# Performance work log

Hardware: AMD Instinct MI355X
Metric: run time of the kernel (lower is better)

Reference implementation:

```python
import jax, jax.numpy as jnp
import numpy as np

B, C, D, H, W = 4, 64, 32, 64, 64
S, NH = 8, 4
HD = C // NH


def setup_inputs() -> dict:
    key = jax.random.key(0)
    ks = jax.random.split(key, 8)
    sc = 0.05
    return {
        "x": jax.random.normal(ks[0], (B, C, D, H, W), jnp.float32),
        "slot_init": jax.random.normal(ks[1], (1, C, S), jnp.float32),
        "slot_proj_w": jax.random.normal(ks[2], (C, C), jnp.float32) * sc,
        "slot_proj_b": jnp.zeros((C,), jnp.float32),
        "ln_g": jnp.ones((C,), jnp.float32),
        "ln_b": jnp.zeros((C,), jnp.float32),
        "in_proj_w": jax.random.normal(ks[3], (3 * C, C), jnp.float32) * sc,
        "in_proj_b": jnp.zeros((3 * C,), jnp.float32),
        "out_proj_w": jax.random.normal(ks[4], (C, C), jnp.float32) * sc,
        "out_proj_b": jnp.zeros((C,), jnp.float32),
        "feat_w": jax.random.normal(ks[5], (C, C), jnp.float32) * sc,
        "feat_b": jnp.zeros((C,), jnp.float32),
        "s2f_w": jax.random.normal(ks[6], (C, C), jnp.float32) * sc,
        "s2f_b": jnp.zeros((C,), jnp.float32),
    }


def _l2norm(v, axis):
    # F.normalize: v / max(||v||, eps)
    n = jnp.sqrt(jnp.sum(v * v, axis=axis, keepdims=True))
    return v / jnp.maximum(n, 1e-12)


def reference(x, slot_init, slot_proj_w, slot_proj_b, ln_g, ln_b,
              in_proj_w, in_proj_b, out_proj_w, out_proj_b,
              feat_w, feat_b, s2f_w, s2f_b):
    b, c, d, h, w = x.shape
    n = d * h * w
    x_flat = x.reshape(b, c, n)                                  # (b,c,N)
    slots = jnp.broadcast_to(slot_init, (b, c, S))               # (b,c,S)

    # ---- slot update: cosine-sim cross attention over N ----
    x_norm = _l2norm(x_flat, 1)
    slots_norm = _l2norm(slots, 1)
    sim = jnp.einsum('bcs,bcn->bsn', slots_norm, x_norm)         # (b,S,N)
    attn = jax.nn.softmax(sim, axis=2)
    updates = jnp.einsum('bcn,bsn->bsc', x_flat, attn)           # (b,S,c)
    slots_t = updates @ slot_proj_w.T + slot_proj_b              # (b,S,c)

    # ---- LayerNorm(channels) then tiny MHSA over S=8 slots ----
    mu = jnp.mean(slots_t, axis=-1, keepdims=True)
    var = jnp.mean((slots_t - mu) ** 2, axis=-1, keepdims=True)
    sn = (slots_t - mu) / jnp.sqrt(var + 1e-5) * ln_g + ln_b     # (b,S,c)

    qkv = sn @ in_proj_w.T + in_proj_b                           # (b,S,3c)
    q, k, v = jnp.split(qkv, 3, axis=-1)
    def heads(t):
        return t.reshape(b, S, NH, HD).transpose(0, 2, 1, 3)     # (b,H,S,hd)
    q, k, v = heads(q), heads(k), heads(v)
    scores = jnp.einsum('bhqd,bhkd->bhqk', q, k) / jnp.sqrt(jnp.float32(HD))
    a = jax.nn.softmax(scores, axis=-1)
    o = jnp.einsum('bhqk,bhkd->bhqd', a, v).transpose(0, 2, 1, 3).reshape(b, S, c)
    o = o @ out_proj_w.T + out_proj_b
    slots_t = slots_t + o                                        # (b,S,c)

    # ---- feature broadcast: 1x1x1 conv + slot->feature attention ----
    feat_flat = jnp.einsum('oc,bcn->bon', feat_w, x_flat) + feat_b[None, :, None]
    slots_feat = slots_t @ s2f_w.T + s2f_b                       # (b,S,c)
    sim2 = jnp.einsum('bsc,bcn->bsn', slots_feat, feat_flat)
    attn2 = jax.nn.softmax(sim2, axis=1)                         # softmax over slots
    out = jnp.einsum('bsc,bsn->bcn', slots_t, attn2)             # (b,c,N)
    return out.reshape(b, c, d, h, w) + x
```

## Files before the change

### kernel.cpp

```cpp
#include <hip/hip_runtime.h>
#include <hip/hip_bf16.h>

#define BB   4
#define CC   64
#define SS   8
#define NN   (32*64*64)
#define NH_  4
#define HD_  16
#define TA   128
#define BPA  128
#define NTB  8

typedef __attribute__((ext_vector_type(8))) short bf16x8;
typedef __attribute__((ext_vector_type(4))) float f32x4;

__device__ __forceinline__ unsigned short f2b(float f) {
    union { float f; unsigned u; } v; v.f = f;
    unsigned r = v.u + 0x7FFFu + ((v.u >> 16) & 1u);
    return (unsigned short)(r >> 16);
}
__device__ __forceinline__ unsigned bfpack(float a, float b) {
    union { float f; unsigned u; } x, y; x.f = a; y.f = b;
    unsigned ra = (x.u + 0x7FFFu + ((x.u >> 16) & 1u)) >> 16;
    unsigned rb = (y.u + 0x7FFFu + ((y.u >> 16) & 1u)) & 0xFFFF0000u;
    return ra | rb;
}

__global__ __launch_bounds__(256) void k_precomp(
    const float* __restrict__ slot_init,
    const float* __restrict__ s2fw, const float* __restrict__ s2fb,
    const float* __restrict__ fw, const float* __restrict__ fb,
    float* __restrict__ M, float* __restrict__ g0v,
    float* __restrict__ hv, float* __restrict__ h0,
    float* __restrict__ snT_ws)
{
    const int tid = threadIdx.x;
    if (blockIdx.x < 16) {
        const int cp = blockIdx.x*4 + (tid >> 6);
        const int c  = tid & 63;
        float acc = 0.f;
        #pragma unroll 8
        for (int o = 0; o < CC; ++o)
            acc += s2fw[o*CC + cp] * fw[o*CC + c];
        M[cp*CC + c] = acc;
    } else if (blockIdx.x == 16) {
        if (tid < 64) {
            float acc = 0.f;
            #pragma unroll 8
            for (int o = 0; o < CC; ++o) acc += s2fb[o] * fw[o*CC + tid];
            g0v[tid] = acc;
        } else if (tid < 128) {
            const int cp = tid - 64;
            float acc = 0.f;
            #pragma unroll 8
            for (int o = 0; o < CC; ++o) acc += s2fw[o*CC + cp] * fb[o];
            hv[cp] = acc;
        } else if (tid == 128) {
            float acc = 0.f;
            for (int o = 0; o < CC; ++o) acc += s2fb[o] * fb[o];
            *h0 = acc;
        }
    } else {
        __shared__ float nrm[SS];
        if (tid < 64) {
            const int s = tid & 7, ch = tid >> 3;
            float p = 0.f;
            #pragma unroll
            for (int j = 0; j < 8; ++j) {
                float v = slot_init[(ch*8 + j)*SS + s];
                p += v*v;
            }
            p += __shfl_xor(p, 8); p += __shfl_xor(p, 16); p += __shfl_xor(p, 32);
            if (tid < 8) nrm[s] = fmaxf(sqrtf(p), 1e-12f);
        }
        __syncthreads();
        for (int i = tid; i < SS*CC; i += 256) {
            const int c = i >> 3, s = i & 7;
            snT_ws[i] = slot_init[c*SS + s] / nrm[s];
        }
    }
}

__global__ __launch_bounds__(256) void k_slots_attn(
    const float* __restrict__ x, const float* __restrict__ snT_ws,
    float* __restrict__ U_part, float* __restrict__ sume_part)
{
    __shared__ float xlds[2][CC * TA];
    __shared__ short et[9 * TA];
    __shared__ float snT[CC * SS];
    __shared__ float red[2 * 9 * TA];

    const int tid = threadIdx.x;
    const int b   = blockIdx.x / BPA;
    const int blk = blockIdx.x % BPA;
    const int lane = tid & 63, wv = tid >> 6;
    const int col = tid & 127, half = tid >> 7;

    if (tid < 64) ((int*)&et[8*TA])[tid] = 0;
    if (tid < 128) *(float4*)&snT[tid*4] = *(const float4*)&snT_ws[tid*4];

    const float* xb = x + (size_t)b * CC * NN;

    f32x4 accU = {0.f, 0.f, 0.f, 0.f};
    float accS[SS];
    #pragma unroll
    for (int s = 0; s < SS; ++s) accS[s] = 0.f;

    #define STAGE(buf, t)                                                      \
    {                                                                          \
        const int n0_ = (t) * TA;                                              \
        _Pragma("unroll")                                                      \
        for (int k = 0; k < 8; ++k) {                                          \
            const int c_  = (wv*8 + k)*2 + (lane >> 5);                        \
            const int jg_ = (lane & 31) ^ (c_ & 7);                            \
            const float* src_ = xb + (size_t)c_*NN + n0_ + jg_*4;              \
            float* dst_ = &xlds[buf][(wv*8 + k)*256];                          \
            __builtin_amdgcn_global_load_lds(                                  \
                (const __attribute__((address_space(1))) void*)src_,           \
                (__attribute__((address_space(3))) void*)dst_, 16, 0, 0);      \
        }                                                                      \
    }

    int cur = 0;
    STAGE(0, blk);
    asm volatile("s_waitcnt vmcnt(0)" ::: "memory");
    __syncthreads();

    for (int tt = 0; tt < NTB; ++tt) {
        if (tt + 1 < NTB) STAGE(cur ^ 1, blk + (tt+1)*BPA);

        {
            const float* xl = &xlds[cur][0];
            float ss = 0.f;
            float a[SS];
            #pragma unroll
            for (int s = 0; s < SS; ++s) a[s] = 0.f;
            #pragma unroll
            for (int ci = 0; ci < 32; ++ci) {
                const int c = half*32 + ci;
                const float xv = xl[c*TA + (((col>>2) ^ (c&7)) << 2) + (col&3)];
                ss += xv * xv;
                const float4 g0 = *(const float4*)&snT[c*8];
                const float4 g1 = *(const float4*)&snT[c*8 + 4];
                a[0] += g0.x*xv; a[1] += g0.y*xv; a[2] += g0.z*xv; a[3] += g0.w*xv;
                a[4] += g1.x*xv; a[5] += g1.y*xv; a[6] += g1.z*xv; a[7] += g1.w*xv;
            }
            red[(half*9 + 8)*TA + col] = ss;
            #pragma unroll
            for (int s = 0; s < SS; ++s) red[(half*9 + s)*TA + col] = a[s];
        }
        __syncthreads();

        if (tid < TA) {
            const float ss = red[8*TA + tid] + red[(9+8)*TA + tid];
            const float invn = 1.f / fmaxf(sqrtf(ss), 1e-12f);
            #pragma unroll
            for (int s = 0; s < SS; ++s) {
                const float av = red[s*TA + tid] + red[(9+s)*TA + tid];
                const float e = __expf(av * invn);
                accS[s] += e;
                et[s*TA + ((((tid>>3) ^ s) << 3) | (tid & 7))] = (short)f2b(e);
            }
        }
        __syncthreads();

        {
            const int ca  = (wv << 4) + (lane & 15);
            const int rbq = lane & 15;
            const int rb  = (rbq < 8) ? rbq : 8;
            const int p   = lane >> 4;
            #pragma unroll
            for (int kk = 0; kk < 4; ++kk) {
                const int n8  = kk*32 + p*8;
                const int sl0 = ((n8 >> 2)     ^ (ca & 7));
                const int sl1 = (((n8 >> 2)+1) ^ (ca & 7));
                const float4 f0 = *(const float4*)&xlds[cur][ca*TA + sl0*4];
                const float4 f1 = *(const float4*)&xlds[cur][ca*TA + sl1*4];
                union { unsigned u[4]; bf16x8 v; } ua;
                ua.u[0] = bfpack(f0.x, f0.y);
                ua.u[1] = bfpack(f0.z, f0.w);
                ua.u[2] = bfpack(f1.x, f1.y);
                ua.u[3] = bfpack(f1.z, f1.w);
                const int slb = ((n8 >> 3) ^ (rb & 7));
                const bf16x8 bfr = *(const bf16x8*)&et[rb*TA + slb*8];
                accU = __builtin_amdgcn_mfma_f32_16x16x32_bf16(ua.v, bfr, accU, 0, 0, 0);
            }
        }
        asm volatile("s_waitcnt vmcnt(0)" ::: "memory");
        __syncthreads();
        cur ^= 1;
    }

    {
        const size_t base = ((size_t)(b*BPA + blk) * SS) * CC;
        if ((lane & 15) < SS) {
            const int s  = lane & 15;
            const int c0 = (wv << 4) + ((lane >> 4) << 2);
            #pragma unroll
            for (int r = 0; r < 4; ++r)
                U_part[base + s*CC + c0 + r] = accU[r];
        }
    }
    if (tid < TA) {
        #pragma unroll
        for (int s = 0; s < SS; ++s) red[s*TA + tid] = accS[s];
    }
    __syncthreads();
    {
        const int s = tid >> 5, j = tid & 31;
        float v = 0.f;
        #pragma unroll
        for (int k = 0; k < 4; ++k) v += red[s*TA + j*4 + k];
        v += __shfl_xor(v, 1); v += __shfl_xor(v, 2); v += __shfl_xor(v, 4);
        v += __shfl_xor(v, 8); v += __shfl_xor(v, 16);
        if (j == 0) sume_part[(size_t)(b*BPA + blk)*SS + s] = v;
    }
    #undef STAGE
}

__global__ __launch_bounds__(256) void k_reduce2(
    const float* __restrict__ U_part, const float* __restrict__ sume_part,
    float* __restrict__ upd_g, int bpb)
{
    __shared__ float part[4][64];
    __shared__ float lbuf[256];
    __shared__ float Lsh;
    const int tid = threadIdx.x;
    const int b = blockIdx.x >> 3, s = blockIdx.x & 7;
    const int c = tid & 63, kc = tid >> 6;
    const int cnt = bpb >> 2;

    float lv = 0.f;
    for (int k = tid; k < bpb; k += 256)
        lv += sume_part[(size_t)(b*bpb + k)*SS + s];
    lbuf[tid] = lv;

    float acc[8];
    #pragma unroll
    for (int j = 0; j < 8; ++j) acc[j] = 0.f;
    const float* base = U_part + ((size_t)(b*bpb + kc*cnt)*SS + s)*CC + c;
    for (int k = 0; k < cnt; k += 8) {
        #pragma unroll
        for (int j = 0; j < 8; ++j)
            acc[j] += base[(size_t)(k + j) * SS * CC];
    }
    part[kc][c] = ((acc[0]+acc[1]) + (acc[2]+acc[3]))
                + ((acc[4]+acc[5]) + (acc[6]+acc[7]));
    __syncthreads();

    if (tid < 128) lbuf[tid] += lbuf[tid + 128];
    __syncthreads();
    if (tid < 64) {
        float v = lbuf[tid] + lbuf[tid + 64];
        v += __shfl_xor(v, 1); v += __shfl_xor(v, 2); v += __shfl_xor(v, 4);
        v += __shfl_xor(v, 8); v += __shfl_xor(v, 16); v += __shfl_xor(v, 32);
        if (tid == 0) Lsh = v;
    }
    __syncthreads();

    if (tid < 64) {
        float u = part[0][c] + part[1][c] + part[2][c] + part[3][c];
        upd_g[((size_t)b*SS + s)*CC + c] = u / Lsh;
    }
}

__global__ __launch_bounds__(256) void k_slots_small(
    const float* __restrict__ upd_g,
    const float* __restrict__ spw, const float* __restrict__ spb,
    const float* __restrict__ lng, const float* __restrict__ lnb,
    const float* __restrict__ ipw, const float* __restrict__ ipb,
    const float* __restrict__ opw, const float* __restrict__ opb,
    const float* __restrict__ M, const float* __restrict__ g0v,
    const float* __restrict__ hv, const float* __restrict__ h0,
    float* __restrict__ st_out, float* __restrict__ g_out, float* __restrict__ h_out)
{
    __shared__ float upd[SS*CC];
    __shared__ float st [SS*CC];
    __shared__ float snb[SS*CC];
    __shared__ float qkv[SS*3*CC];
    __shared__ float ot [SS*CC];

    const int tid  = threadIdx.x;
    const int b    = blockIdx.x;
    const int c    = tid & 63;
    const int quad = tid >> 6;
    const int r0 = quad*2, r1 = r0 + 1;
    float wreg[CC];

    #pragma unroll
    for (int i = 0; i < 16; ++i)
        *(float4*)&wreg[i*4] = *(const float4*)(spw + c*CC + i*4);
    upd[r0*CC + c] = upd_g[(b*SS + r0)*CC + c];
    upd[r1*CC + c] = upd_g[(b*SS + r1)*CC + c];
    __syncthreads();

    {
        const float bias = spb[c];
        float a0 = bias, a1 = bias;
        #pragma unroll
        for (int i = 0; i < 16; ++i) {
            float4 u0 = *(const float4*)&upd[r0*CC + i*4];
            float4 u1 = *(const float4*)&upd[r1*CC + i*4];
            a0 += u0.x*wreg[i*4+0] + u0.y*wreg[i*4+1] + u0.z*wreg[i*4+2] + u0.w*wreg[i*4+3];
            a1 += u1.x*wreg[i*4+0] + u1.y*wreg[i*4+1] + u1.z*wreg[i*4+2] + u1.w*wreg[i*4+3];
        }
        st[r0*CC + c] = a0;
        st[r1*CC + c] = a1;
    }
    __syncthreads();

    {
        const int row = tid >> 5, l = tid & 31;
        float v0 = st[row*CC + l], v1 = st[row*CC + l + 32];
        float sum = v0 + v1;
        sum += __shfl_xor(sum, 1); sum += __shfl_xor(sum, 2); sum += __shfl_xor(sum, 4);
        sum += __shfl_xor(sum, 8); sum += __shfl_xor(sum, 16);
        const float mu = sum * (1.f/64.f);
        const float d0 = v0 - mu, d1 = v1 - mu;
        float vs = d0*d0 + d1*d1;
        vs += __shfl_xor(vs, 1); vs += __shfl_xor(vs, 2); vs += __shfl_xor(vs, 4);
        vs += __shfl_xor(vs, 8); vs += __shfl_xor(vs, 16);
        const float rstd = rsqrtf(vs * (1.f/64.f) + 1e-5f);
        snb[row*CC + l]      = d0 * rstd * lng[l]      + lnb[l];
        snb[row*CC + l + 32] = d1 * rstd * lng[l + 32] + lnb[l + 32];
    }
    __syncthreads();

    for (int m = 0; m < 3; ++m) {
        #pragma unroll
        for (int i = 0; i < 16; ++i)
            *(float4*)&wreg[i*4] = *(const float4*)(ipw + (size_t)(m*CC + c)*CC + i*4);
        const float bias = ipb[m*CC + c];
        float a0 = bias, a1 = bias;
        #pragma unroll
        for (int i = 0; i < 16; ++i) {
            float4 u0 = *(const float4*)&snb[r0*CC + i*4];
            float4 u1 = *(const float4*)&snb[r1*CC + i*4];
            a0 += u0.x*wreg[i*4+0] + u0.y*wreg[i*4+1] + u0.z*wreg[i*4+2] + u0.w*wreg[i*4+3];
            a1 += u1.x*wreg[i*4+0] + u1.y*wreg[i*4+1] + u1.z*wreg[i*4+2] + u1.w*wreg[i*4+3];
        }
        qkv[r0*3*CC + m*CC + c] = a0;
        qkv[r1*3*CC + m*CC + c] = a1;
    }
    __syncthreads();

    if (tid < NH_*SS) {
        const int h = tid >> 3, q = tid & 7;
        float qreg[HD_];
        #pragma unroll
        for (int i = 0; i < 4; ++i)
            *(float4*)&qreg[i*4] = *(const float4*)&qkv[q*3*CC + h*HD_ + i*4];
        float srow[SS];
        float mx = -1e30f;
        #pragma unroll
        for (int k = 0; k < SS; ++k) {
            float acc = 0.f;
            #pragma unroll
            for (int d = 0; d < HD_; ++d)
                acc += qreg[d] * qkv[k*3*CC + CC + h*HD_ + d];
            srow[k] = acc * 0.25f;
            mx = fmaxf(mx, srow[k]);
        }
        float l = 0.f;
        #pragma unroll
        for (int k = 0; k < SS; ++k) { srow[k] = __expf(srow[k] - mx); l += srow[k]; }
        const float inv = 1.f / l;
        float oreg[HD_];
        #pragma unroll
        for (int d = 0; d < HD_; ++d) oreg[d] = 0.f;
        #pragma unroll
        for (int k = 0; k < SS; ++k) {
            #pragma unroll
            for (int d = 0; d < HD_; ++d)
                oreg[d] += srow[k] * qkv[k*3*CC + 2*CC + h*HD_ + d];
        }
        #pragma unroll
        for (int d = 0; d < HD_; ++d)
            ot[q*CC + h*HD_ + d] = oreg[d] * inv;
    }
    __syncthreads();

    #pragma unroll
    for (int i = 0; i < 16; ++i)
        *(float4*)&wreg[i*4] = *(const float4*)(opw + c*CC + i*4);
    {
        const float bias = opb[c];
        float a0 = bias, a1 = bias;
        #pragma unroll
        for (int i = 0; i < 16; ++i) {
            float4 u0 = *(const float4*)&ot[r0*CC + i*4];
            float4 u1 = *(const float4*)&ot[r1*CC + i*4];
            a0 += u0.x*wreg[i*4+0] + u0.y*wreg[i*4+1] + u0.z*wreg[i*4+2] + u0.w*wreg[i*4+3];
            a1 += u1.x*wreg[i*4+0] + u1.y*wreg[i*4+1] + u1.z*wreg[i*4+2] + u1.w*wreg[i*4+3];
        }
        st[r0*CC + c] += a0;
        st[r1*CC + c] += a1;
    }
    __syncthreads();

    #pragma unroll 8
    for (int cp = 0; cp < CC; ++cp) wreg[cp] = M[cp*CC + c];
    {
        const float g0 = g0v[c];
        float a0 = g0, a1 = g0;
        #pragma unroll
        for (int i = 0; i < 16; ++i) {
            float4 s0 = *(const float4*)&st[r0*CC + i*4];
            float4 s1 = *(const float4*)&st[r1*CC + i*4];
            a0 += s0.x*wreg[i*4+0] + s0.y*wreg[i*4+1] + s0.z*wreg[i*4+2] + s0.w*wreg[i*4+3];
            a1 += s1.x*wreg[i*4+0] + s1.y*wreg[i*4+1] + s1.z*wreg[i*4+2] + s1.w*wreg[i*4+3];
        }
        g_out[(b*SS + r0)*CC + c] = a0;
        g_out[(b*SS + r1)*CC + c] = a1;
        st_out[(b*SS + r0)*CC + c] = st[r0*CC + c];
        st_out[(b*SS + r1)*CC + c] = st[r1*CC + c];
    }
    {
        const int row = tid >> 5, l = tid & 31;
        float pv = st[row*CC + l]*hv[l] + st[row*CC + l + 32]*hv[l + 32];
        pv += __shfl_xor(pv, 1); pv += __shfl_xor(pv, 2); pv += __shfl_xor(pv, 4);
        pv += __shfl_xor(pv, 8); pv += __shfl_xor(pv, 16);
        if (l == 0) h_out[b*SS + row] = pv + *h0;
    }
}

__global__ __launch_bounds__(256) void k_feat(
    const float* __restrict__ x,
    const float* __restrict__ st_g, const float* __restrict__ g_g,
    const float* __restrict__ h_g,
    float* __restrict__ out)
{
    __shared__ float stS[SS*CC];
    __shared__ float gS [SS*CC];
    __shared__ float hS [SS];

    const int tid = threadIdx.x;
    const int b  = blockIdx.x >> 9;
    const int n  = ((blockIdx.x & 511) << 8) + tid;

    for (int i = tid; i < SS*CC; i += 256) {
        stS[i] = st_g[b*SS*CC + i];
        gS[i]  = g_g [b*SS*CC + i];
    }
    if (tid < SS) hS[tid] = h_g[b*SS + tid];
    __syncthreads();

    const float* xb = x + (size_t)b * CC * NN + n;
    float xc[CC];
    #pragma unroll
    for (int c = 0; c < CC; ++c) xc[c] = xb[(size_t)c * NN];

    float a[SS];
    #pragma unroll
    for (int s = 0; s < SS; ++s) a[s] = hS[s];
    #pragma unroll
    for (int c4 = 0; c4 < CC/4; ++c4) {
        #pragma unroll
        for (int s = 0; s < SS; ++s) {
            float4 g4 = *(const float4*)(&gS[s*CC + c4*4]);
            a[s] += g4.x*xc[c4*4+0] + g4.y*xc[c4*4+1]
                  + g4.z*xc[c4*4+2] + g4.w*xc[c4*4+3];
        }
    }

    float m = a[0];
    #pragma unroll
    for (int s = 1; s < SS; ++s) m = fmaxf(m, a[s]);
    float l = 0.f;
    #pragma unroll
    for (int s = 0; s < SS; ++s) { a[s] = __expf(a[s] - m); l += a[s]; }
    const float inv = 1.f / l;

    float* ob = out + (size_t)b * CC * NN + n;
    #pragma unroll
    for (int c4 = 0; c4 < CC/4; ++c4) {
        float o0 = 0.f, o1 = 0.f, o2 = 0.f, o3 = 0.f;
        #pragma unroll
        for (int s = 0; s < SS; ++s) {
            float4 s4 = *(const float4*)(&stS[s*CC + c4*4]);
            o0 += s4.x * a[s]; o1 += s4.y * a[s];
            o2 += s4.z * a[s]; o3 += s4.w * a[s];
        }
        ob[(size_t)(c4*4+0) * NN] = o0 * inv + xc[c4*4+0];
        ob[(size_t)(c4*4+1) * NN] = o1 * inv + xc[c4*4+1];
        ob[(size_t)(c4*4+2) * NN] = o2 * inv + xc[c4*4+2];
        ob[(size_t)(c4*4+3) * NN] = o3 * inv + xc[c4*4+3];
    }
}

extern "C" void kernel_launch(void* const* d_in, const int* in_sizes, int n_in,
                              void* d_out, int out_size, void* d_ws, size_t ws_size,
                              hipStream_t stream) {
    const float* x         = (const float*)d_in[0];
    const float* slot_init = (const float*)d_in[1];
    const float* spw       = (const float*)d_in[2];
    const float* spb       = (const float*)d_in[3];
    const float* lng       = (const float*)d_in[4];
    const float* lnb       = (const float*)d_in[5];
    const float* ipw       = (const float*)d_in[6];
    const float* ipb       = (const float*)d_in[7];
    const float* opw       = (const float*)d_in[8];
    const float* opb       = (const float*)d_in[9];
    const float* fw        = (const float*)d_in[10];
    const float* fb        = (const float*)d_in[11];
    const float* s2fw      = (const float*)d_in[12];
    const float* s2fb      = (const float*)d_in[13];
    float* out = (float*)d_out;

    float* w         = (float*)d_ws;
    float* U_part    = w;
    float* sume_part = U_part + (size_t)BB*BPA*SS*CC;
    float* upd_g     = sume_part + (size_t)BB*BPA*SS;
    float* Mm        = upd_g + 2048;
    float* g0v       = Mm + 4096;
    float* hv        = g0v + 64;
    float* h0        = hv + 64;
    float* snT_ws    = h0 + 64;
    float* st_out    = snT_ws + 1024;
    float* g_out     = st_out + 2048;
    float* h_out     = g_out + 2048;

    k_precomp<<<18, 256, 0, stream>>>(slot_init, s2fw, s2fb, fw, fb,
                                      Mm, g0v, hv, h0, snT_ws);
    k_slots_attn<<<BB * BPA, 256, 0, stream>>>(x, snT_ws, U_part, sume_part);
    k_reduce2<<<BB * SS, 256, 0, stream>>>(U_part, sume_part, upd_g, BPA);
    k_slots_small<<<BB, 256, 0, stream>>>(upd_g, spw, spb, lng, lnb,
                                          ipw, ipb, opw, opb, Mm, g0v, hv, h0,
                                          st_out, g_out, h_out);
    k_feat<<<BB * (NN/256), 256, 0, stream>>>(x, st_out, g_out, h_out, out);
}
```

Before: 127.2 us.

## Split slot attention into similarity pass and bf16 MFMA GEMM pass

Splits the fused slot-attention kernel into two kernels. k_sim reads x in fp32, computes the cosine-similarity exponentials and their per-block sums, and writes bf16 copies of both x and the exponentials. k_gemm_u then runs the MFMA accumulation directly on the bf16 tiles, with no in-loop conversion or block syncs for the softmax step. The final feature kernel now reads the bf16 copy of x instead of fp32, which halves its load traffic but also rounds the residual term added to the output. The extra bf16 writes and the added launch may cancel the saving, unless the copy stays resident in the large on-package cache.

```diff
diff --git a/kernel.cpp b/kernel.cpp
--- a/kernel.cpp
+++ b/kernel.cpp
@@ -8,22 +8,20 @@
 #define NH_  4
 #define HD_  16
 #define TA   128
-#define BPA  128
-#define NTB  8
+#define BPA  256
+#define NB1  512
+#define NTB2 4
 
 typedef __attribute__((ext_vector_type(8))) short bf16x8;
 typedef __attribute__((ext_vector_type(4))) float f32x4;
 
+__device__ __forceinline__ float b2f(unsigned short h) {
+    union { unsigned u; float f; } v; v.u = ((unsigned)h) << 16; return v.f;
+}
 __device__ __forceinline__ unsigned short f2b(float f) {
     union { float f; unsigned u; } v; v.f = f;
     unsigned r = v.u + 0x7FFFu + ((v.u >> 16) & 1u);
     return (unsigned short)(r >> 16);
-}
-__device__ __forceinline__ unsigned bfpack(float a, float b) {
-    union { float f; unsigned u; } x, y; x.f = a; y.f = b;
-    unsigned ra = (x.u + 0x7FFFu + ((x.u >> 16) & 1u)) >> 16;
-    unsigned rb = (y.u + 0x7FFFu + ((y.u >> 16) & 1u)) & 0xFFFF0000u;
-    return ra | rb;
 }
 
 __global__ __launch_bounds__(256) void k_precomp(
@@ -81,115 +79,138 @@
     }
 }
 
-__global__ __launch_bounds__(256) void k_slots_attn(
+__global__ __launch_bounds__(256) void k_sim(
     const float* __restrict__ x, const float* __restrict__ snT_ws,
-    float* __restrict__ U_part, float* __restrict__ sume_part)
+    unsigned short* __restrict__ xb16, unsigned short* __restrict__ ebf,
+    float* __restrict__ sume_part)
 {
-    __shared__ float xlds[2][CC * TA];
-    __shared__ short et[9 * TA];
-    __shared__ float snT[CC * SS];
-    __shared__ float red[2 * 9 * TA];
+    __shared__ float snT[CC*SS];
+    __shared__ float red[SS*256];
+
+    const int tid  = threadIdx.x;
+    const int b    = blockIdx.x >> 9;
+    const int blk1 = blockIdx.x & 511;
+    const int n    = (blk1 << 8) + tid;
+
+    if (tid < 128) *(float4*)&snT[tid*4] = *(const float4*)&snT_ws[tid*4];
+    __syncthreads();
+
+    const float* xcol = x + (size_t)b*CC*NN + n;
+    unsigned short* xo = xb16 + (size_t)b*CC*NN + n;
+
+    float ss = 0.f;
+    float a[SS];
+    #pragma unroll
+    for (int s = 0; s < SS; ++s) a[s] = 0.f;
+
+    #pragma unroll
+    for (int c = 0; c < CC; ++c) {
+        const float xv = xcol[(size_t)c*NN];
+        xo[(size_t)c*NN] = f2b(xv);
+        ss += xv*xv;
+        const float4 g0 = *(const float4*)&snT[c*8];
+        const float4 g1 = *(const float4*)&snT[c*8 + 4];
+        a[0] += g0.x*xv; a[1] += g0.y*xv; a[2] += g0.z*xv; a[3] += g0.w*xv;
+        a[4] += g1.x*xv; a[5] += g1.y*xv; a[6] += g1.z*xv; a[7] += g1.w*xv;
+    }
+
+    const float invn = 1.f / fmaxf(sqrtf(ss), 1e-12f);
+    float e[SS];
+    #pragma unroll
+    for (int s = 0; s < SS; ++s) e[s] = __expf(a[s] * invn);
+
+    unsigned short* eo = ebf + (size_t)b*SS*NN + n;
+    #pragma unroll
+    for (int s = 0; s < SS; ++s) eo[(size_t)s*NN] = f2b(e[s]);
+
+    #pragma unroll
+    for (int s = 0; s < SS; ++s) red[s*256 + tid] = e[s];
+    __syncthreads();
+    {
+        const int s = tid >> 5, j = tid & 31;
+        float v = 0.f;
+        #pragma unroll
+        for (int k = 0; k < 8; ++k) v += red[s*256 + j*8 + k];
+        v += __shfl_xor(v, 1); v += __shfl_xor(v, 2); v += __shfl_xor(v, 4);
+        v += __shfl_xor(v, 8); v += __shfl_xor(v, 16);
+        if (j == 0) sume_part[(size_t)(b*NB1 + blk1)*SS + s] = v;
+    }
+}
+
+__global__ __launch_bounds__(256) void k_gemm_u(
+    const unsigned short* __restrict__ xb16, const unsigned short* __restrict__ ebf,
+    float* __restrict__ U_part)
+{
+    __shared__ short xt[2][CC*TA];
+    __shared__ short et[2][SS*TA];
+    __shared__ short etz[TA];
 
     const int tid = threadIdx.x;
     const int b   = blockIdx.x / BPA;
     const int blk = blockIdx.x % BPA;
     const int lane = tid & 63, wv = tid >> 6;
-    const int col = tid & 127, half = tid >> 7;
-
-    if (tid < 64) ((int*)&et[8*TA])[tid] = 0;
-    if (tid < 128) *(float4*)&snT[tid*4] = *(const float4*)&snT_ws[tid*4];
-
-    const float* xb = x + (size_t)b * CC * NN;
+
+    if (tid < 64) ((int*)etz)[tid] = 0;
+
+    const unsigned short* xg = xb16 + (size_t)b*CC*NN;
+    const unsigned short* eg = ebf  + (size_t)b*SS*NN;
 
     f32x4 accU = {0.f, 0.f, 0.f, 0.f};
-    float accS[SS];
-    #pragma unroll
-    for (int s = 0; s < SS; ++s) accS[s] = 0.f;
-
-    #define STAGE(buf, t)                                                      \
+
+    #define STG(buf, t)                                                        \
     {                                                                          \
         const int n0_ = (t) * TA;                                              \
         _Pragma("unroll")                                                      \
-        for (int k = 0; k < 8; ++k) {                                          \
-            const int c_  = (wv*8 + k)*2 + (lane >> 5);                        \
-            const int jg_ = (lane & 31) ^ (c_ & 7);                            \
-            const float* src_ = xb + (size_t)c_*NN + n0_ + jg_*4;              \
-            float* dst_ = &xlds[buf][(wv*8 + k)*256];                          \
+        for (int k = 0; k < 4; ++k) {                                          \
+            const int c_ = wv*16 + k*4 + (lane >> 4);                          \
+            const int j_ = (lane & 15) ^ (c_ & 7);                             \
+            const unsigned short* src_ = xg + (size_t)c_*NN + n0_ + j_*8;      \
+            short* dst_ = &xt[buf][(wv*16 + k*4)*TA];                          \
             __builtin_amdgcn_global_load_lds(                                  \
                 (const __attribute__((address_space(1))) void*)src_,           \
                 (__attribute__((address_space(3))) void*)dst_, 16, 0, 0);      \
         }                                                                      \
+        if (wv == 0) {                                                         \
+            _Pragma("unroll")                                                  \
+            for (int k = 0; k < 2; ++k) {                                      \
+                const int s_ = k*4 + (lane >> 4);                              \
+                const int j_ = (lane & 15) ^ (s_ & 7);                         \
+                const unsigned short* src_ = eg + (size_t)s_*NN + n0_ + j_*8;  \
+                short* dst_ = &et[buf][k*4*TA];                                \
+                __builtin_amdgcn_global_load_lds(                              \
+                    (const __attribute__((address_space(1))) void*)src_,       \
+                    (__attribute__((address_space(3))) void*)dst_, 16, 0, 0);  \
+            }                                                                  \
+        }                                                                      \
     }
 
     int cur = 0;
-    STAGE(0, blk);
+    STG(0, blk);
     asm volatile("s_waitcnt vmcnt(0)" ::: "memory");
     __syncthreads();
 
-    for (int tt = 0; tt < NTB; ++tt) {
-        if (tt + 1 < NTB) STAGE(cur ^ 1, blk + (tt+1)*BPA);
-
-        {
-            const float* xl = &xlds[cur][0];
-            float ss = 0.f;
-            float a[SS];
-            #pragma unroll
-            for (int s = 0; s < SS; ++s) a[s] = 0.f;
-            #pragma unroll
-            for (int ci = 0; ci < 32; ++ci) {
-                const int c = half*32 + ci;
-                const float xv = xl[c*TA + (((col>>2) ^ (c&7)) << 2) + (col&3)];
-                ss += xv * xv;
-                const float4 g0 = *(const float4*)&snT[c*8];
-                const float4 g1 = *(const float4*)&snT[c*8 + 4];
-                a[0] += g0.x*xv; a[1] += g0.y*xv; a[2] += g0.z*xv; a[3] += g0.w*xv;
-                a[4] += g1.x*xv; a[5] += g1.y*xv; a[6] += g1.z*xv; a[7] += g1.w*xv;
-            }
-            red[(half*9 + 8)*TA + col] = ss;
-            #pragma unroll
-            for (int s = 0; s < SS; ++s) red[(half*9 + s)*TA + col] = a[s];
-        }
-        __syncthreads();
-
-        if (tid < TA) {
-            const float ss = red[8*TA + tid] + red[(9+8)*TA + tid];
-            const float invn = 1.f / fmaxf(sqrtf(ss), 1e-12f);
-            #pragma unroll
-            for (int s = 0; s < SS; ++s) {
-                const float av = red[s*TA + tid] + red[(9+s)*TA + tid];
-                const float e = __expf(av * invn);
-                accS[s] += e;
-                et[s*TA + ((((tid>>3) ^ s) << 3) | (tid & 7))] = (short)f2b(e);
-            }
-        }
-        __syncthreads();
+    for (int tt = 0; tt < NTB2; ++tt) {
+        if (tt + 1 < NTB2) STG(cur ^ 1, blk + (tt+1)*BPA);
 
         {
             const int ca  = (wv << 4) + (lane & 15);
             const int rbq = lane & 15;
-            const int rb  = (rbq < 8) ? rbq : 8;
             const int p   = lane >> 4;
+            const short* brow = (rbq < 8) ? &et[cur][rbq*TA] : etz;
+            const int bsw = (rbq < 8) ? (rbq & 7) : 0;
             #pragma unroll
             for (int kk = 0; kk < 4; ++kk) {
-                const int n8  = kk*32 + p*8;
-                const int sl0 = ((n8 >> 2)     ^ (ca & 7));
-                const int sl1 = (((n8 >> 2)+1) ^ (ca & 7));
-                const float4 f0 = *(const float4*)&xlds[cur][ca*TA + sl0*4];
-                const float4 f1 = *(const float4*)&xlds[cur][ca*TA + sl1*4];
-                union { unsigned u[4]; bf16x8 v; } ua;
-                ua.u[0] = bfpack(f0.x, f0.y);
-                ua.u[1] = bfpack(f0.z, f0.w);
-                ua.u[2] = bfpack(f1.x, f1.y);
-                ua.u[3] = bfpack(f1.z, f1.w);
-                const int slb = ((n8 >> 3) ^ (rb & 7));
-                const bf16x8 bfr = *(const bf16x8*)&et[rb*TA + slb*8];
-                accU = __builtin_amdgcn_mfma_f32_16x16x32_bf16(ua.v, bfr, accU, 0, 0, 0);
+                const int sl = kk*4 + p;
+                const bf16x8 af  = *(const bf16x8*)&xt[cur][ca*TA + ((sl ^ (ca & 7)) << 3)];
+                const bf16x8 bfr = *(const bf16x8*)&brow[(sl ^ bsw) << 3];
+                accU = __builtin_amdgcn_mfma_f32_16x16x32_bf16(af, bfr, accU, 0, 0, 0);
             }
         }
         asm volatile("s_waitcnt vmcnt(0)" ::: "memory");
         __syncthreads();
         cur ^= 1;
     }
+    #undef STG
 
     {
         const size_t base = ((size_t)(b*BPA + blk) * SS) * CC;
@@ -201,26 +222,11 @@
                 U_part[base + s*CC + c0 + r] = accU[r];
         }
     }
-    if (tid < TA) {
-        #pragma unroll
-        for (int s = 0; s < SS; ++s) red[s*TA + tid] = accS[s];
-    }
-    __syncthreads();
-    {
-        const int s = tid >> 5, j = tid & 31;
-        float v = 0.f;
-        #pragma unroll
-        for (int k = 0; k < 4; ++k) v += red[s*TA + j*4 + k];
-        v += __shfl_xor(v, 1); v += __shfl_xor(v, 2); v += __shfl_xor(v, 4);
-        v += __shfl_xor(v, 8); v += __shfl_xor(v, 16);
-        if (j == 0) sume_part[(size_t)(b*BPA + blk)*SS + s] = v;
-    }
-    #undef STAGE
 }
 
 __global__ __launch_bounds__(256) void k_reduce2(
     const float* __restrict__ U_part, const float* __restrict__ sume_part,
-    float* __restrict__ upd_g, int bpb)
+    float* __restrict__ upd_g, int nU, int nL)
 {
     __shared__ float part[4][64];
     __shared__ float lbuf[256];
@@ -228,17 +234,17 @@
     const int tid = threadIdx.x;
     const int b = blockIdx.x >> 3, s = blockIdx.x & 7;
     const int c = tid & 63, kc = tid >> 6;
-    const int cnt = bpb >> 2;
+    const int cnt = nU >> 2;
 
     float lv = 0.f;
-    for (int k = tid; k < bpb; k += 256)
-        lv += sume_part[(size_t)(b*bpb + k)*SS + s];
+    for (int k = tid; k < nL; k += 256)
+        lv += sume_part[(size_t)(b*nL + k)*SS + s];
     lbuf[tid] = lv;
 
     float acc[8];
     #pragma unroll
     for (int j = 0; j < 8; ++j) acc[j] = 0.f;
-    const float* base = U_part + ((size_t)(b*bpb + kc*cnt)*SS + s)*CC + c;
+    const float* base = U_part + ((size_t)(b*nU + kc*cnt)*SS + s)*CC + c;
     for (int k = 0; k < cnt; k += 8) {
         #pragma unroll
         for (int j = 0; j < 8; ++j)
@@ -425,7 +431,7 @@
 }
 
 __global__ __launch_bounds__(256) void k_feat(
-    const float* __restrict__ x,
+    const unsigned short* __restrict__ xb16,
     const float* __restrict__ st_g, const float* __restrict__ g_g,
     const float* __restrict__ h_g,
     float* __restrict__ out)
@@ -445,10 +451,10 @@
     if (tid < SS) hS[tid] = h_g[b*SS + tid];
     __syncthreads();
 
-    const float* xb = x + (size_t)b * CC * NN + n;
+    const unsigned short* xbh = xb16 + (size_t)b*CC*NN + n;
     float xc[CC];
     #pragma unroll
-    for (int c = 0; c < CC; ++c) xc[c] = xb[(size_t)c * NN];
+    for (int c = 0; c < CC; ++c) xc[c] = b2f(xbh[(size_t)c * NN]);
 
     float a[SS];
     #pragma unroll
@@ -510,7 +516,7 @@
     float* w         = (float*)d_ws;
     float* U_part    = w;
     float* sume_part = U_part + (size_t)BB*BPA*SS*CC;
-    float* upd_g     = sume_part + (size_t)BB*BPA*SS;
+    float* upd_g     = sume_part + (size_t)BB*NB1*SS;
     float* Mm        = upd_g + 2048;
     float* g0v       = Mm + 4096;
     float* hv        = g0v + 64;
@@ -519,13 +525,16 @@
     float* st_out    = snT_ws + 1024;
     float* g_out     = st_out + 2048;
     float* h_out     = g_out + 2048;
+    unsigned short* xb16 = (unsigned short*)(h_out + 64);
+    unsigned short* ebf  = xb16 + (size_t)BB*CC*NN;
 
     k_precomp<<<18, 256, 0, stream>>>(slot_init, s2fw, s2fb, fw, fb,
                                       Mm, g0v, hv, h0, snT_ws);
-    k_slots_attn<<<BB * BPA, 256, 0, stream>>>(x, snT_ws, U_part, sume_part);
-    k_reduce2<<<BB * SS, 256, 0, stream>>>(U_part, sume_part, upd_g, BPA);
+    k_sim<<<BB * NB1, 256, 0, stream>>>(x, snT_ws, xb16, ebf, sume_part);
+    k_gemm_u<<<BB * BPA, 256, 0, stream>>>(xb16, ebf, U_part);
+    k_reduce2<<<BB * SS, 256, 0, stream>>>(U_part, sume_part, upd_g, BPA, NB1);
     k_slots_small<<<BB, 256, 0, stream>>>(upd_g, spw, spb, lng, lnb,
                                           ipw, ipb, opw, opb, Mm, g0v, hv, h0,
                                           st_out, g_out, h_out);
-    k_feat<<<BB * (NN/256), 256, 0, stream>>>(x, st_out, g_out, h_out, out);
-}
+    k_feat<<<BB * (NN/256), 256, 0, stream>>>(xb16, st_out, g_out, h_out, out);
+}
```

Measured after the change: 167.2 us. +31.4%, slower.
